# Optimization experiments

Hardware: AMD Instinct MI355X
Metric: run time of the kernel (lower is better)

## Reference

```python
import jax, jax.numpy as jnp
import numpy as np

B, T, H, L = 64, 2048, 256, 16


def setup_inputs() -> dict:
    key = jax.random.key(0)
    ks = jax.random.split(key, 6)
    x = jax.random.normal(ks[0], (B, T, H), dtype=jnp.float32)
    tags = jax.random.randint(ks[1], (B, T), 0, L).astype(jnp.int32)
    mask = jnp.ones((B, T), dtype=bool)  # torchcrf requires mask[:,0] all on
    W = jax.random.normal(ks[2], (L, H), dtype=jnp.float32) * (1.0 / np.sqrt(H))
    b = jnp.zeros((L,), dtype=jnp.float32)
    # torchcrf initializes transitions ~ U(-0.1, 0.1)
    start_transitions = jax.random.uniform(ks[3], (L,), minval=-0.1, maxval=0.1)
    end_transitions = jax.random.uniform(ks[4], (L,), minval=-0.1, maxval=0.1)
    transitions = jax.random.uniform(ks[5], (L, L), minval=-0.1, maxval=0.1)
    return {"x": x, "W": W, "b": b,
            "start_transitions": start_transitions,
            "end_transitions": end_transitions,
            "transitions": transitions,
            "tags": tags, "mask": mask}


def reference(x, W, b, start_transitions, end_transitions, transitions, tags, mask):
    # Emitter: Linear(hidden_dim -> num_labels)
    emissions = jnp.einsum('bth,lh->btl', x, W) + b  # [B,T,L]
    maskf = mask.astype(emissions.dtype)             # [B,T]

    # ---- numerator: score of the gold tag path (vectorized, no scan) ----
    emit_gold = jnp.take_along_axis(emissions, tags[..., None].astype(jnp.int32), axis=2)[..., 0]  # [B,T]
    first_tags = tags[:, 0]
    score = start_transitions[first_tags] + emit_gold[:, 0]
    trans_gold = transitions[tags[:, :-1], tags[:, 1:]]  # [B,T-1]
    score = score + jnp.sum((trans_gold + emit_gold[:, 1:]) * maskf[:, 1:], axis=1)
    seq_ends = jnp.sum(mask.astype(jnp.int32), axis=1) - 1  # index of last valid step
    last_tags = jnp.take_along_axis(tags, seq_ends[:, None], axis=1)[:, 0]
    score = score + end_transitions[last_tags]

    # ---- denominator: forward algorithm (log partition) via lax.scan over time ----
    em_t = jnp.swapaxes(emissions, 0, 1)  # [T,B,L]
    mask_t = jnp.swapaxes(mask, 0, 1)     # [T,B]
    alpha0 = start_transitions[None, :] + em_t[0]  # [B,L]

    def step(alpha, inp):
        em, m = inp  # em: [B,L], m: [B]
        # logsumexp over previous label: alpha[b,i] + transitions[i,j] + em[b,j]
        nxt = jax.nn.logsumexp(alpha[:, :, None] + transitions[None, :, :] + em[:, None, :], axis=1)
        alpha = jnp.where(m[:, None], nxt, alpha)
        return alpha, None

    alphaT, _ = jax.lax.scan(step, alpha0, (em_t[1:], mask_t[1:]))
    denom = jax.nn.logsumexp(alphaT + end_transitions[None, :], axis=1)  # [B]

    llh = score - denom          # log-likelihood per sequence
    return -jnp.mean(llh)        # reduction='mean', nll = -crf(...)
```

## Files before the change

kernel.cpp:

```cpp
#include <hip/hip_runtime.h>
#include <math.h>


#define Bb 64
#define Tt 2048
#define Hh 256
#define Ll 16
#define CHUNK 32
#define NC (Tt / CHUNK)
#define ROWS 128
#define TSTR 20

typedef __attribute__((ext_vector_type(8))) short short8;
typedef __attribute__((ext_vector_type(4))) short short4v;
typedef __attribute__((ext_vector_type(4))) float f32x4;

__device__ __forceinline__ unsigned pk2bf(float a, float b) {
  unsigned ua = __float_as_uint(a) + 0x8000u;
  unsigned ub = __float_as_uint(b) + 0x8000u;
  return (ua >> 16) | (ub & 0xFFFF0000u);
}
__device__ __forceinline__ short8 pack8(float4 lo, float4 hi) {
  union { int4 i; short8 s; } u;
  u.i.x = pk2bf(lo.x, lo.y);
  u.i.y = pk2bf(lo.z, lo.w);
  u.i.z = pk2bf(hi.x, hi.y);
  u.i.w = pk2bf(hi.z, hi.w);
  return u.s;
}

#if __has_builtin(__builtin_amdgcn_mfma_f32_16x16x16bf16_1k)
#define MFMA16(a, b, c) __builtin_amdgcn_mfma_f32_16x16x16bf16_1k(a, b, c, 0, 0, 0)
#else
__device__ __forceinline__ f32x4 mfma16_asm(short4v a, short4v b, f32x4 c) {
  f32x4 d;
  asm("v_mfma_f32_16x16x16_bf16 %0, %1, %2, %3" : "=v"(d) : "v"(a), "v"(b), "v"(c));
  return d;
}
#define MFMA16(a, b, c) mfma16_asm(a, b, c)
#endif

__device__ __forceinline__ void gload_lds16(const float* g, char* l) {
  __builtin_amdgcn_global_load_lds((const __attribute__((address_space(1))) void*)g,
                                   (__attribute__((address_space(3))) void*)l, 16, 0, 0);
}

__global__ __launch_bounds__(256, 4) void k_fused(const float* __restrict__ x,
                                                  const float* __restrict__ W,
                                                  const float* __restrict__ bias,
                                                  const float* __restrict__ strans,
                                                  const float* __restrict__ etrans,
                                                  const float* __restrict__ trans,
                                                  const int* __restrict__ tags,
                                                  float* __restrict__ em0,
                                                  float* __restrict__ Pout,
                                                  float* __restrict__ lscale,
                                                  float* __restrict__ score) {
  __shared__ __align__(16) char smem[4 * 8192];

  const int tid = threadIdx.x, w = tid >> 6, lane = tid & 63;
  const int n = lane & 15, quad = lane >> 4;
  const int b = blockIdx.x >> 4, blk = blockIdx.x & 15;
  const int gc = blk * 4 + w;
  char* xw = smem + w * 8192;

  f32x4 acc0 = {0.f, 0.f, 0.f, 0.f}, acc1 = {0.f, 0.f, 0.f, 0.f};
  float bs;
  {
    const float4* wp4 = (const float4*)(W + (size_t)n * Hh) + quad * 2;
    float4 wv[16];
#pragma unroll
    for (int ks = 0; ks < 8; ++ks) { wv[2 * ks] = wp4[ks * 8]; wv[2 * ks + 1] = wp4[ks * 8 + 1]; }
    bs = bias[n];

    const size_t R0 = (size_t)blockIdx.x * ROWS + (size_t)w * 32;
    const int gsel = (lane & 7) ^ ((lane >> 3) & 7);
    const float* srcb = x + (R0 + (size_t)(lane >> 3)) * Hh + gsel * 4;

#define STAGEI(cc, bb) { \
      const float* sp_ = srcb + (cc) * 32; \
      char* lb_ = xw + (bb) * 4096; \
      gload_lds16(sp_,           lb_); \
      gload_lds16(sp_ + 8 * Hh,  lb_ + 1024); \
      gload_lds16(sp_ + 16 * Hh, lb_ + 2048); \
      gload_lds16(sp_ + 24 * Hh, lb_ + 3072); }

    STAGEI(0, 0)
    STAGEI(1, 1)

    short8 Bf[8];
#pragma unroll
    for (int ks = 0; ks < 8; ++ks) Bf[ks] = pack8(wv[2 * ks], wv[2 * ks + 1]);

    const int r7 = n & 7;
    const unsigned o0 = (unsigned)(((2 * quad) ^ r7) << 4);
    const unsigned o1 = (unsigned)(((2 * quad + 1) ^ r7) << 4);
    const unsigned rowb = (unsigned)(n * 128);

#pragma unroll
    for (int c = 0; c < 8; ++c) {
      if (c < 7) { asm volatile("s_waitcnt vmcnt(4)" ::: "memory"); }
      else       { asm volatile("s_waitcnt vmcnt(0)" ::: "memory"); }
      __builtin_amdgcn_sched_barrier(0);
      const char* rb = xw + (c & 1) * 4096;
      float4 v0 = *(const float4*)(rb + rowb + o0);
      float4 v1 = *(const float4*)(rb + rowb + o1);
      float4 u0 = *(const float4*)(rb + 2048 + rowb + o0);
      float4 u1 = *(const float4*)(rb + 2048 + rowb + o1);
      short8 a0 = pack8(v0, v1);
      short8 a1 = pack8(u0, u1);
      acc0 = __builtin_amdgcn_mfma_f32_16x16x32_bf16(a0, Bf[c], acc0, 0, 0, 0);
      acc1 = __builtin_amdgcn_mfma_f32_16x16x32_bf16(a1, Bf[c], acc1, 0, 0, 0);
      if (c + 2 < 8) STAGEI(c + 2, c & 1)
    }
#undef STAGEI
  }

  float* emw = (float*)xw;
  {
#pragma unroll
    for (int r = 0; r < 4; ++r) {
      emw[(quad * 4 + r) * TSTR + n] = acc0[r] + bs;
      emw[(16 + quad * 4 + r) * TSTR + n] = acc1[r] + bs;
    }
    if (blk == 0 && w == 0 && quad == 0) em0[b * 16 + n] = acc0[0] + bs;
  }

  {
    float s2 = 0.f;
    if (lane < 32) {
      int rl = lane;
      int t = blk * ROWS + w * 32 + rl;
      int gt = b * Tt + t;
      int tag = tags[gt];
      float ev = emw[rl * TSTR + tag];
      if (t == 0) s2 = strans[tag] + ev;
      else        s2 = trans[tags[gt - 1] * 16 + tag] + ev;
      if (t == Tt - 1) s2 += etrans[tag];
    }
#pragma unroll
    for (int msk = 1; msk < 64; msk <<= 1) s2 += __shfl_xor(s2, msk);
    if (lane == 0) atomicAdd(score + b, s2);
  }

  unsigned short* ghb = (unsigned short*)(xw + 2560);
  float offsum = 0.f;
  {
    if (lane < 32) {
      int rl = lane;
      const float4* tp = (const float4*)(emw + rl * TSTR);
      float4 a0 = tp[0], a1 = tp[1], a2 = tp[2], a3 = tp[3];
      float m = fmaxf(fmaxf(fmaxf(fmaxf(a0.x, a0.y), fmaxf(a0.z, a0.w)),
                            fmaxf(fmaxf(a1.x, a1.y), fmaxf(a1.z, a1.w))),
                      fmaxf(fmaxf(fmaxf(a2.x, a2.y), fmaxf(a2.z, a2.w)),
                            fmaxf(fmaxf(a3.x, a3.y), fmaxf(a3.z, a3.w))));
      float4 e0 = make_float4(expf(a0.x - m), expf(a0.y - m), expf(a0.z - m), expf(a0.w - m));
      float4 e1 = make_float4(expf(a1.x - m), expf(a1.y - m), expf(a1.z - m), expf(a1.w - m));
      float4 e2 = make_float4(expf(a2.x - m), expf(a2.y - m), expf(a2.z - m), expf(a2.w - m));
      float4 e3 = make_float4(expf(a3.x - m), expf(a3.y - m), expf(a3.z - m), expf(a3.w - m));
      int4 lo, hi;
      lo.x = pk2bf(e0.x, e0.y); lo.y = pk2bf(e0.z, e0.w);
      lo.z = pk2bf(e1.x, e1.y); lo.w = pk2bf(e1.z, e1.w);
      hi.x = pk2bf(e2.x, e2.y); hi.y = pk2bf(e2.z, e2.w);
      hi.z = pk2bf(e3.x, e3.y); hi.w = pk2bf(e3.z, e3.w);
      ((int4*)ghb)[rl * 2] = lo;
      ((int4*)ghb)[rl * 2 + 1] = hi;
      int t = blk * ROWS + w * 32 + rl;
      offsum = (t >= 1) ? m : 0.f;
    }
#pragma unroll
    for (int msk = 1; msk < 64; msk <<= 1) offsum += __shfl_xor(offsum, msk);
  }

  {
    union { unsigned u[2]; short4v s4; } ae;
    {
      float e0 = 0.25f * expf(trans[(quad * 4 + 0) * 16 + n]);
      float e1 = 0.25f * expf(trans[(quad * 4 + 1) * 16 + n]);
      float e2 = 0.25f * expf(trans[(quad * 4 + 2) * 16 + n]);
      float e3 = 0.25f * expf(trans[(quad * 4 + 3) * 16 + n]);
      ae.u[0] = pk2bf(e0, e1);
      ae.u[1] = pk2bf(e2, e3);
    }
    union { unsigned u[2]; short sh[4]; short4v s4; } bq;
    bq.u[0] = 0; bq.u[1] = 0;
    if ((n >> 2) == quad) bq.sh[n & 3] = (short)0x3F80;

    const int sbeg = (gc == 0) ? 1 : 0;
    const unsigned short* grow = ghb + quad * 4;
    short4v Bq = bq.s4;
    f32x4 d;
#define PSTEP(ss) { \
      const unsigned* gp = (const unsigned*)(grow + (ss) * 16); \
      unsigned glo = gp[0], ghi = gp[1]; \
      f32x4 z = {0.f, 0.f, 0.f, 0.f}; \
      d = MFMA16(ae.s4, Bq, z); \
      d[0] *= __uint_as_float(glo << 16); \
      d[1] *= __uint_as_float(glo & 0xFFFF0000u); \
      d[2] *= __uint_as_float(ghi << 16); \
      d[3] *= __uint_as_float(ghi & 0xFFFF0000u); \
      union { unsigned pu[2]; short4v ps; } pb; \
      pb.pu[0] = pk2bf(d[0], d[1]); \
      pb.pu[1] = pk2bf(d[2], d[3]); \
      Bq = pb.ps; }
    if (sbeg == 0) PSTEP(0)
#pragma unroll
    for (int s = 1; s < CHUNK; ++s) PSTEP(s)
#undef PSTEP

    float mx = fmaxf(fmaxf(d[0], d[1]), fmaxf(d[2], d[3]));
#pragma unroll
    for (int msk = 1; msk < 64; msk <<= 1) mx = fmaxf(mx, __shfl_xor(mx, msk));
    float inv = __builtin_amdgcn_rcpf(mx);
    float off = offsum + (float)(CHUNK - sbeg) * 1.3862943611198906f + logf(mx);

    float* Pw = (float*)(xw + 3584);
#pragma unroll
    for (int r = 0; r < 4; ++r) Pw[n * TSTR + quad * 4 + r] = d[r] * inv;
    {
      int i = lane >> 2, jg = lane & 3;
      float4 pv = *(const float4*)(Pw + i * TSTR + jg * 4);
      ((float4*)(Pout + ((size_t)(b * NC + gc)) * 256))[lane] = pv;
      if (lane == 0) lscale[b * NC + gc] = off;
    }
  }
}

__global__ __launch_bounds__(256) void k_combine(const float* __restrict__ em0,
                                                 const float* __restrict__ P,
                                                 const float* __restrict__ lscale,
                                                 const float* __restrict__ strans,
                                                 const float* __restrict__ etrans,
                                                 float* __restrict__ denom) {
  int b = blockIdx.x, tid = threadIdx.x;
  __shared__ float Pl[NC * 256];
  const float4* src = (const float4*)(P + (size_t)b * NC * 256);
  float4* dst = (float4*)Pl;
  for (int idx = tid; idx < NC * 64; idx += 256) dst[idx] = src[idx];
  __syncthreads();
  if (tid >= 64) return;
  int lane = tid;
  float ls = lscale[b * NC + lane];
#pragma unroll
  for (int m = 1; m < 64; m <<= 1) ls += __shfl_xor(ls, m);

  int j = lane & 15, ig = lane >> 4;
  float a = strans[j] + em0[b * 16 + j];
  float m0 = a;
#pragma unroll
  for (int m = 1; m < 16; m <<= 1) m0 = fmaxf(m0, __shfl_xor(m0, m));
  float v = expf(a - m0);
  float o = m0 + ls;

  for (int cc = 0; cc < NC; ++cc) {
    const float* Pc = Pl + cc * 256;
    float part = 0.f;
#pragma unroll
    for (int r = 0; r < 4; ++r) {
      int srcl = (ig << 4) + ig * 4 + r;
      float vr = __shfl(v, srcl);
      part = fmaf(vr, Pc[(ig * 4 + r) * 16 + j], part);
    }
    part += __shfl_xor(part, 16);
    part += __shfl_xor(part, 32);
    if ((cc & 3) == 3) {
      float mx = part;
#pragma unroll
      for (int m = 1; m < 16; m <<= 1) mx = fmaxf(mx, __shfl_xor(mx, m));
      o += logf(mx);
      v = part * __builtin_amdgcn_rcpf(mx);
    } else {
      v = part;
    }
  }
  float sj = v * expf(etrans[j]);
#pragma unroll
  for (int m = 1; m < 16; m <<= 1) sj += __shfl_xor(sj, m);
  if (lane == 0) denom[b] = o + logf(sj);
}

__global__ __launch_bounds__(64) void k_final(const float* __restrict__ score,
                                              const float* __restrict__ denom,
                                              float* __restrict__ out) {
  int lane = threadIdx.x;
  float llh = score[lane] - denom[lane];
#pragma unroll
  for (int m = 1; m < 64; m <<= 1) llh += __shfl_xor(llh, m);
  if (lane == 0) out[0] = -llh * (1.0f / 64.0f);
}

extern "C" void kernel_launch(void* const* d_in, const int* in_sizes, int n_in,
                              void* d_out, int out_size, void* d_ws, size_t ws_size,
                              hipStream_t stream) {
  const float* x = (const float*)d_in[0];
  const float* W = (const float*)d_in[1];
  const float* bias = (const float*)d_in[2];
  const float* strans = (const float*)d_in[3];
  const float* etrans = (const float*)d_in[4];
  const float* trans = (const float*)d_in[5];
  const int* tags = (const int*)d_in[6];

  float* ws = (float*)d_ws;
  float* em0 = ws;
  float* P = em0 + Bb * 16;
  float* lscale = P + (size_t)Bb * NC * 256;
  float* score = lscale + Bb * NC;
  float* denom = score + Bb;
  float* out = (float*)d_out;

  hipMemsetAsync(score, 0, Bb * sizeof(float), stream);
  hipLaunchKernelGGL(k_fused, dim3(Bb * Tt / ROWS), dim3(256), 0, stream,
                     x, W, bias, strans, etrans, trans, tags, em0, P, lscale, score);
  hipLaunchKernelGGL(k_combine, dim3(Bb), dim3(256), 0, stream, em0, P, lscale, strans, etrans, denom);
  hipLaunchKernelGGL(k_final, dim3(1), dim3(64), 0, stream, score, denom, out);
}
```

Baseline: 242.9 us.

## Use one chunk per block: all warps stage x, wave 0 computes

Each block previously had 4 waves, each processing its own 32-row chunk with a double-buffered global_load_lds pipeline. Now each block handles a single 32-row chunk. All 4 waves cooperatively load the whole 32x256 tile into LDS, then waves 1-3 exit and wave 0 runs the MFMA projection and the chunk scan. This quadruples the block count and spreads the load issue across all waves. In exchange, it gives up the overlap of loads with compute, idles three waves during the serial scan, and raises LDS use per block to about 36KB, which may limit occupancy.

```diff
diff --git a/kernel.cpp b/kernel.cpp
--- a/kernel.cpp
+++ b/kernel.cpp
@@ -8,7 +8,6 @@
 #define Ll 16
 #define CHUNK 32
 #define NC (Tt / CHUNK)
-#define ROWS 128
 #define TSTR 20
 
 typedef __attribute__((ext_vector_type(8))) short short8;
@@ -56,81 +55,77 @@
                                                   float* __restrict__ Pout,
                                                   float* __restrict__ lscale,
                                                   float* __restrict__ score) {
-  __shared__ __align__(16) char smem[4 * 8192];
+  __shared__ __align__(16) char stage[32 * 1024];
+  __shared__ float emw[CHUNK * TSTR];
+  __shared__ unsigned short ghb[CHUNK * 16];
+  __shared__ float Pbuf[16 * TSTR];
 
   const int tid = threadIdx.x, w = tid >> 6, lane = tid & 63;
   const int n = lane & 15, quad = lane >> 4;
-  const int b = blockIdx.x >> 4, blk = blockIdx.x & 15;
-  const int gc = blk * 4 + w;
-  char* xw = smem + w * 8192;
+  const int b = blockIdx.x >> 6, gc = blockIdx.x & 63;
+
+  {
+    const size_t R0 = (size_t)blockIdx.x * CHUNK;
+#pragma unroll
+    for (int i = 0; i < 8; ++i) {
+      const int r = w * 8 + i;
+      const float* src = x + (R0 + (size_t)r) * Hh + ((lane ^ (r & 7)) * 4);
+      gload_lds16(src, stage + r * 1024);
+    }
+  }
+  __syncthreads();
+  if (w != 0) return;
 
   f32x4 acc0 = {0.f, 0.f, 0.f, 0.f}, acc1 = {0.f, 0.f, 0.f, 0.f};
-  float bs;
-  {
-    const float4* wp4 = (const float4*)(W + (size_t)n * Hh) + quad * 2;
-    float4 wv[16];
-#pragma unroll
-    for (int ks = 0; ks < 8; ++ks) { wv[2 * ks] = wp4[ks * 8]; wv[2 * ks + 1] = wp4[ks * 8 + 1]; }
-    bs = bias[n];
-
-    const size_t R0 = (size_t)blockIdx.x * ROWS + (size_t)w * 32;
-    const int gsel = (lane & 7) ^ ((lane >> 3) & 7);
-    const float* srcb = x + (R0 + (size_t)(lane >> 3)) * Hh + gsel * 4;
-
-#define STAGEI(cc, bb) { \
-      const float* sp_ = srcb + (cc) * 32; \
-      char* lb_ = xw + (bb) * 4096; \
-      gload_lds16(sp_,           lb_); \
-      gload_lds16(sp_ + 8 * Hh,  lb_ + 1024); \
-      gload_lds16(sp_ + 16 * Hh, lb_ + 2048); \
-      gload_lds16(sp_ + 24 * Hh, lb_ + 3072); }
-
-    STAGEI(0, 0)
-    STAGEI(1, 1)
-
+  const float bs = bias[n];
+  {
+    const float* wbase = W + (size_t)n * Hh + quad * 8;
     short8 Bf[8];
 #pragma unroll
-    for (int ks = 0; ks < 8; ++ks) Bf[ks] = pack8(wv[2 * ks], wv[2 * ks + 1]);
+    for (int bt = 0; bt < 2; ++bt) {
+      float4 wv[8];
+#pragma unroll
+      for (int c2 = 0; c2 < 4; ++c2) {
+        const int c = bt * 4 + c2;
+        wv[2 * c2]     = *(const float4*)(wbase + c * 32);
+        wv[2 * c2 + 1] = *(const float4*)(wbase + c * 32 + 4);
+      }
+#pragma unroll
+      for (int c2 = 0; c2 < 4; ++c2) Bf[bt * 4 + c2] = pack8(wv[2 * c2], wv[2 * c2 + 1]);
+    }
 
     const int r7 = n & 7;
-    const unsigned o0 = (unsigned)(((2 * quad) ^ r7) << 4);
-    const unsigned o1 = (unsigned)(((2 * quad + 1) ^ r7) << 4);
-    const unsigned rowb = (unsigned)(n * 128);
-
+    const unsigned o0 = (unsigned)((((2 * quad) ^ r7)) << 4);
+    const unsigned o1 = (unsigned)((((2 * quad + 1) ^ r7)) << 4);
+    const char* row0 = stage + n * 1024;
+    const char* row1 = stage + (n + 16) * 1024;
 #pragma unroll
     for (int c = 0; c < 8; ++c) {
-      if (c < 7) { asm volatile("s_waitcnt vmcnt(4)" ::: "memory"); }
-      else       { asm volatile("s_waitcnt vmcnt(0)" ::: "memory"); }
-      __builtin_amdgcn_sched_barrier(0);
-      const char* rb = xw + (c & 1) * 4096;
-      float4 v0 = *(const float4*)(rb + rowb + o0);
-      float4 v1 = *(const float4*)(rb + rowb + o1);
-      float4 u0 = *(const float4*)(rb + 2048 + rowb + o0);
-      float4 u1 = *(const float4*)(rb + 2048 + rowb + o1);
+      float4 v0 = *(const float4*)(row0 + 128 * c + o0);
+      float4 v1 = *(const float4*)(row0 + 128 * c + o1);
+      float4 u0 = *(const float4*)(row1 + 128 * c + o0);
+      float4 u1 = *(const float4*)(row1 + 128 * c + o1);
       short8 a0 = pack8(v0, v1);
       short8 a1 = pack8(u0, u1);
       acc0 = __builtin_amdgcn_mfma_f32_16x16x32_bf16(a0, Bf[c], acc0, 0, 0, 0);
       acc1 = __builtin_amdgcn_mfma_f32_16x16x32_bf16(a1, Bf[c], acc1, 0, 0, 0);
-      if (c + 2 < 8) STAGEI(c + 2, c & 1)
-    }
-#undef STAGEI
-  }
-
-  float* emw = (float*)xw;
+    }
+  }
+
   {
 #pragma unroll
     for (int r = 0; r < 4; ++r) {
       emw[(quad * 4 + r) * TSTR + n] = acc0[r] + bs;
       emw[(16 + quad * 4 + r) * TSTR + n] = acc1[r] + bs;
     }
-    if (blk == 0 && w == 0 && quad == 0) em0[b * 16 + n] = acc0[0] + bs;
+    if (gc == 0 && quad == 0) em0[b * 16 + n] = acc0[0] + bs;
   }
 
   {
     float s2 = 0.f;
     if (lane < 32) {
       int rl = lane;
-      int t = blk * ROWS + w * 32 + rl;
+      int t = gc * CHUNK + rl;
       int gt = b * Tt + t;
       int tag = tags[gt];
       float ev = emw[rl * TSTR + tag];
@@ -143,7 +138,6 @@
     if (lane == 0) atomicAdd(score + b, s2);
   }
 
-  unsigned short* ghb = (unsigned short*)(xw + 2560);
   float offsum = 0.f;
   {
     if (lane < 32) {
@@ -165,7 +159,7 @@
       hi.z = pk2bf(e3.x, e3.y); hi.w = pk2bf(e3.z, e3.w);
       ((int4*)ghb)[rl * 2] = lo;
       ((int4*)ghb)[rl * 2 + 1] = hi;
-      int t = blk * ROWS + w * 32 + rl;
+      int t = gc * CHUNK + rl;
       offsum = (t >= 1) ? m : 0.f;
     }
 #pragma unroll
@@ -214,12 +208,11 @@
     float inv = __builtin_amdgcn_rcpf(mx);
     float off = offsum + (float)(CHUNK - sbeg) * 1.3862943611198906f + logf(mx);
 
-    float* Pw = (float*)(xw + 3584);
-#pragma unroll
-    for (int r = 0; r < 4; ++r) Pw[n * TSTR + quad * 4 + r] = d[r] * inv;
+#pragma unroll
+    for (int r = 0; r < 4; ++r) Pbuf[n * TSTR + quad * 4 + r] = d[r] * inv;
     {
       int i = lane >> 2, jg = lane & 3;
-      float4 pv = *(const float4*)(Pw + i * TSTR + jg * 4);
+      float4 pv = *(const float4*)(Pbuf + i * TSTR + jg * 4);
       ((float4*)(Pout + ((size_t)(b * NC + gc)) * 256))[lane] = pv;
       if (lane == 0) lscale[b * NC + gc] = off;
     }
@@ -309,7 +302,7 @@
   float* out = (float*)d_out;
 
   hipMemsetAsync(score, 0, Bb * sizeof(float), stream);
-  hipLaunchKernelGGL(k_fused, dim3(Bb * Tt / ROWS), dim3(256), 0, stream,
+  hipLaunchKernelGGL(k_fused, dim3(Bb * NC), dim3(256), 0, stream,
                      x, W, bias, strans, etrans, trans, tags, em0, P, lscale, score);
   hipLaunchKernelGGL(k_combine, dim3(Bb), dim3(256), 0, stream, em0, P, lscale, strans, etrans, denom);
   hipLaunchKernelGGL(k_final, dim3(1), dim3(64), 0, stream, score, denom, out);
```

Result: no change. 243.8 us (+0.4%).
